# Kernel tuning notes

Measured on AMD Instinct MI355X. Metric: run time of the kernel, lower is better.

Reference implementation:

```python
import jax, jax.numpy as jnp
import numpy as np

B, S, DIN = 4, 2048, 1024
H, D = 16, 64  # num_head, per-head dim_out


def _xavier(key, shape):
    fan_in, fan_out = shape[0], shape[1]
    limit = float(np.sqrt(6.0 / (fan_in + fan_out)))
    return jax.random.uniform(key, shape, jnp.float32, -limit, limit)


def setup_inputs() -> dict:
    key = jax.random.key(0)
    k_x, k_q, k_k, k_v, k_o = jax.random.split(key, 5)
    inputs = jax.random.normal(k_x, (B, S, DIN), jnp.float32)
    # weights stored as [in, out] (transpose of torch Linear.weight); bias zeros
    return {
        "inputs": inputs,
        "wq": _xavier(k_q, (DIN, H * D)), "bq": jnp.zeros((H * D,), jnp.float32),
        "wk": _xavier(k_k, (DIN, H * D)), "bk": jnp.zeros((H * D,), jnp.float32),
        "wv": _xavier(k_v, (DIN, H * D)), "bv": jnp.zeros((H * D,), jnp.float32),
        "wo": _xavier(k_o, (H * D, D)),  "bo": jnp.zeros((D,), jnp.float32),
    }


def reference(inputs, wq, bq, wk, bk, wv, bv, wo, bo):
    b, s, _ = inputs.shape
    q = (inputs @ wq + bq).reshape(b, s, H, D).transpose(0, 2, 1, 3)  # bhsd
    k = (inputs @ wk + bk).reshape(b, s, H, D).transpose(0, 2, 1, 3)
    v = (inputs @ wv + bv).reshape(b, s, H, D).transpose(0, 2, 1, 3)
    scores = jnp.einsum('bhsd,bhSd->bhsS', q, k) / jnp.sqrt(jnp.float32(D))
    p = jax.nn.softmax(scores, axis=-1)
    o = jnp.einsum('bhsS,bhSd->bhsd', p, v)
    o = o.transpose(0, 2, 1, 3).reshape(b, s, H * D)
    return o @ wo + bo  # [b, s, D]
```

## Files before the change

kernel.cpp:

```cpp
#include <hip/hip_runtime.h>

typedef __attribute__((ext_vector_type(8))) __bf16 bf16x8;
typedef __attribute__((ext_vector_type(4))) float f32x4;

#define NB   4
#define NS   2048
#define NDIN 1024
#define NH   16
#define ND   64
#define NHD  1024
#define NM   (NB * NS)

__device__ __forceinline__ float bf2f(unsigned short u) {
    unsigned int x = ((unsigned int)u) << 16;
    return __builtin_bit_cast(float, x);
}
__device__ __forceinline__ unsigned short f2bf(float f) {
    unsigned int u = __builtin_bit_cast(unsigned int, f);
    u += 0x7fff + ((u >> 16) & 1);
    return (unsigned short)(u >> 16);
}
__device__ __forceinline__ unsigned int cvt_pk_bf16(float lo, float hi) {
    unsigned int r;
    asm("v_cvt_pk_bf16_f32 %0, %1, %2" : "=v"(r) : "v"(lo), "v"(hi));
    return r;
}
__device__ __forceinline__ void gload16(const unsigned short* g, unsigned short* l) {
    __builtin_amdgcn_global_load_lds((const __attribute__((address_space(1))) unsigned int*)g,
                                     (__attribute__((address_space(3))) unsigned int*)l, 16, 0, 0);
}

__global__ __launch_bounds__(256) void prep(
    const float* __restrict__ X, const float* __restrict__ wq,
    const float* __restrict__ wk, const float* __restrict__ wv,
    const float* __restrict__ wo, unsigned short* __restrict__ Xb,
    unsigned short* __restrict__ Wt, unsigned short* __restrict__ WoT) {
    __shared__ unsigned short t[32][33];
    int blk = blockIdx.x, tid = threadIdx.x;
    if (blk < 4096) {
        int i = blk * 256 + tid;
        float4 a = ((const float4*)X)[i * 2];
        float4 b = ((const float4*)X)[i * 2 + 1];
        union { uint4 u; unsigned short s[8]; } o;
        o.s[0] = f2bf(a.x); o.s[1] = f2bf(a.y); o.s[2] = f2bf(a.z); o.s[3] = f2bf(a.w);
        o.s[4] = f2bf(b.x); o.s[5] = f2bf(b.y); o.s[6] = f2bf(b.z); o.s[7] = f2bf(b.w);
        *(uint4*)(Xb + (size_t)i * 8) = o.u;
    } else if (blk < 4096 + 3072) {
        int bb = blk - 4096;
        int z = bb >> 10, rem = bb & 1023;
        const float* src = z == 0 ? wq : z == 1 ? wk : wv;
        unsigned short* dst = Wt + (size_t)z * 1024 * 1024;
        int k0 = (rem & 31) * 32, n0 = (rem >> 5) * 32;
        int tx = tid & 31, ty = tid >> 5;
#pragma unroll
        for (int i = 0; i < 32; i += 8)
            t[ty + i][tx] = f2bf(src[(size_t)(k0 + ty + i) * 1024 + (n0 + tx)]);
        __syncthreads();
#pragma unroll
        for (int i = 0; i < 32; i += 8)
            dst[(size_t)(n0 + ty + i) * 1024 + (k0 + tx)] = t[tx][ty + i];
    } else {
        int bb = blk - 7168;
        int k0 = (bb & 31) * 32, n0 = (bb >> 5) * 32;
        int tx = tid & 31, ty = tid >> 5;
#pragma unroll
        for (int i = 0; i < 32; i += 8)
            t[ty + i][tx] = f2bf(wo[(size_t)(k0 + ty + i) * 64 + (n0 + tx)]);
        __syncthreads();
#pragma unroll
        for (int i = 0; i < 32; i += 8)
            WoT[(size_t)(n0 + ty + i) * 1024 + (k0 + tx)] = t[tx][ty + i];
    }
}

__global__ __launch_bounds__(256) void gemm_qkv(
    const unsigned short* __restrict__ X, const unsigned short* __restrict__ Wt,
    const float* __restrict__ bq, const float* __restrict__ bk,
    const float* __restrict__ bv,
    unsigned short* __restrict__ Q, unsigned short* __restrict__ K,
    unsigned short* __restrict__ V) {
    __shared__ unsigned short smem[16384];

    int lin = blockIdx.x;
    int xcd = lin & 7, ii = lin >> 3;
    int mt = xcd * 8 + (ii & 7);
    int nt = ii >> 3;
    int mb = mt * 128, nb = nt * 128;

    int tid = threadIdx.x;
    int wid = tid >> 6, lane = tid & 63, quad = lane >> 4, l16 = lane & 15;
    int wm = (wid & 1) * 64, wn = (wid >> 1) * 64;

    int srow = 16 * wid + (lane >> 2);
    int scol = (lane & 3) * 8;
    const unsigned short* pa0 = X + (size_t)(mb + srow) * NDIN + scol;
    const unsigned short* pa1 = pa0 + (size_t)64 * NDIN;
    const unsigned short* pb0 = Wt + (size_t)(nb + srow) * NDIN + scol;
    const unsigned short* pb1 = pb0 + (size_t)64 * NDIN;

    auto stage = [&](int buf) {
        unsigned short* la = smem + buf * 8192 + wid * 512;
        unsigned short* lb = smem + buf * 8192 + 4096 + wid * 512;
        gload16(pa0, la);
        gload16(pa1, la + 2048);
        gload16(pb0, lb);
        gload16(pb1, lb + 2048);
        pa0 += 32; pa1 += 32; pb0 += 32; pb1 += 32;
    };

    f32x4 acc[4][4];
#pragma unroll
    for (int i = 0; i < 4; i++)
#pragma unroll
        for (int j = 0; j < 4; j++) acc[i][j] = (f32x4){0.f, 0.f, 0.f, 0.f};

    stage(0);
    __syncthreads();
    int cur = 0;
    for (int k0 = 0; k0 < NDIN; k0 += 32) {
        if (k0 + 32 < NDIN) stage(cur ^ 1);
        const unsigned short* Ab = smem + cur * 8192;
        const unsigned short* Bb = Ab + 4096;
        bf16x8 af[4], bfr[4];
#pragma unroll
        for (int i = 0; i < 4; i++)
            af[i] = *(const bf16x8*)(Ab + (wm + i * 16 + l16) * 32 + quad * 8);
#pragma unroll
        for (int j = 0; j < 4; j++)
            bfr[j] = *(const bf16x8*)(Bb + (wn + j * 16 + l16) * 32 + quad * 8);
#pragma unroll
        for (int i = 0; i < 4; i++)
#pragma unroll
            for (int j = 0; j < 4; j++)
                acc[i][j] = __builtin_amdgcn_mfma_f32_16x16x32_bf16(af[i], bfr[j], acc[i][j], 0, 0, 0);
        __syncthreads();
        cur ^= 1;
    }

    unsigned short (*Cl)[128] = (unsigned short (*)[128])smem;
    int wsel = nb >> 10;
    const float* bias = (wsel == 0) ? bq : (wsel == 1) ? bk : bv;
    unsigned short* dstp = (wsel == 0) ? Q : (wsel == 1) ? K : V;
#pragma unroll
    for (int i = 0; i < 4; i++)
#pragma unroll
        for (int j = 0; j < 4; j++) {
            int nl = wn + j * 16 + l16;
            float bias_v = bias[(nb & 1023) + nl];
#pragma unroll
            for (int r = 0; r < 4; r++) {
                int ml = wm + i * 16 + quad * 4 + r;
                int pc = ((nl >> 3) ^ (ml & 15));
                Cl[ml][(pc << 3) | (nl & 7)] = f2bf(acc[i][j][r] + bias_v);
            }
        }
    __syncthreads();
    {
        int hl = tid >> 7, sl = tid & 127;
        int h = ((nb & 1023) >> 6) + hl;
        int m = mb + sl, b = m >> 11, sidx = m & 2047;
        unsigned short* orow = dstp + ((size_t)((b * NH + h) * NS + sidx)) * ND;
#pragma unroll
        for (int c = 0; c < 8; c++) {
            int pc = ((hl * 8 + c) ^ (sl & 15));
            *(uint4*)(orow + c * 8) = *(const uint4*)(&Cl[sl][pc << 3]);
        }
    }
}

__global__ __launch_bounds__(256) void attn(
    const unsigned short* __restrict__ Q, const unsigned short* __restrict__ K,
    const unsigned short* __restrict__ V, unsigned short* __restrict__ Obuf) {
    __shared__ unsigned short Kl[2][64][64];
    __shared__ unsigned short Vt[2][64][64];

    int lin = blockIdx.x;
    int xcd = lin & 7, idx = lin >> 3;
    int bh = ((idx >> 4) << 3) | xcd;
    int qt = idx & 15;

    size_t base = (size_t)bh * NS * ND;
    int tid = threadIdx.x, wid = tid >> 6, lane = tid & 63;
    int quad = lane >> 4, l16 = lane & 15;
    int lx = l16 & 7;
    int q0 = qt * 128 + wid * 32;

    bf16x8 qa[2][2];
#pragma unroll
    for (int s = 0; s < 2; s++)
#pragma unroll
        for (int f = 0; f < 2; f++) {
            union { uint4 u; unsigned short sv[8]; } in_, out_;
            in_.u = *(const uint4*)(Q + base + (size_t)(q0 + s * 16 + l16) * ND + f * 32 + quad * 8);
#pragma unroll
            for (int j = 0; j < 8; j++) out_.sv[j] = f2bf(bf2f(in_.sv[j]) * 0.125f);
            qa[s][f] = __builtin_bit_cast(bf16x8, out_.u);
        }

    float lrow[2] = {0.f, 0.f};
    f32x4 o[2][4];
#pragma unroll
    for (int s = 0; s < 2; s++)
#pragma unroll
        for (int t = 0; t < 4; t++) o[s][t] = (f32x4){0.f, 0.f, 0.f, 0.f};

    int c0 = tid, c1 = tid + 256;
    int kr0w = c0 >> 3, kc0 = c0 & 7, kg0c = kc0 ^ (kr0w & 7);
    int kr1w = c1 >> 3, kc1 = c1 & 7, kg1c = kc1 ^ (kr1w & 7);
    const unsigned short* kp0 = K + base + (size_t)kr0w * ND + kc0 * 8;
    const unsigned short* kp1 = K + base + (size_t)kr1w * ND + kc1 * 8;
    int p = tid & 31, dqA = tid >> 5, dqB = dqA + 8;
    int cp = ((p >> 4) << 2) | ((p >> 1) & 3);
    int ps = (((p >> 3) & 1) << 2) | ((p & 1) << 1);
    int cb = cp ^ ((dqA & 1) << 2);
    const unsigned short* vg = V + base + (size_t)(2 * p) * ND + dqA * 4;

    uint4 k0r, k1r;
    uint2 va0, va1, va2, va3;

    auto loadRegs = [&]() {
        k0r = *(const uint4*)kp0;
        k1r = *(const uint4*)kp1;
        va0 = *(const uint2*)(vg);
        va1 = *(const uint2*)(vg + ND);
        va2 = *(const uint2*)(vg + 32);
        va3 = *(const uint2*)(vg + ND + 32);
    };
    auto bump = [&]() { kp0 += 64 * ND; kp1 += 64 * ND; vg += 64 * ND; };

    auto writeKV = [&](int buf) {
        *(uint4*)(&Kl[buf][kr0w][kg0c * 8]) = k0r;
        *(uint4*)(&Kl[buf][kr1w][kg1c * 8]) = k1r;
        unsigned short* vt = &Vt[buf][0][0];
        unsigned int w0 = __builtin_amdgcn_perm(va1.x, va0.x, 0x05040100u);
        unsigned int w1 = __builtin_amdgcn_perm(va1.x, va0.x, 0x07060302u);
        unsigned int w2 = __builtin_amdgcn_perm(va1.y, va0.y, 0x05040100u);
        unsigned int w3 = __builtin_amdgcn_perm(va1.y, va0.y, 0x07060302u);
        *(unsigned int*)(vt + (dqA * 4 + 0) * 64 + ((cb ^ 0) << 3) + ps) = w0;
        *(unsigned int*)(vt + (dqA * 4 + 1) * 64 + ((cb ^ 1) << 3) + ps) = w1;
        *(unsigned int*)(vt + (dqA * 4 + 2) * 64 + ((cb ^ 2) << 3) + ps) = w2;
        *(unsigned int*)(vt + (dqA * 4 + 3) * 64 + ((cb ^ 3) << 3) + ps) = w3;
        unsigned int x0 = __builtin_amdgcn_perm(va3.x, va2.x, 0x05040100u);
        unsigned int x1 = __builtin_amdgcn_perm(va3.x, va2.x, 0x07060302u);
        unsigned int x2 = __builtin_amdgcn_perm(va3.y, va2.y, 0x05040100u);
        unsigned int x3 = __builtin_amdgcn_perm(va3.y, va2.y, 0x07060302u);
        *(unsigned int*)(vt + (dqB * 4 + 0) * 64 + ((cb ^ 0) << 3) + ps) = x0;
        *(unsigned int*)(vt + (dqB * 4 + 1) * 64 + ((cb ^ 1) << 3) + ps) = x1;
        *(unsigned int*)(vt + (dqB * 4 + 2) * 64 + ((cb ^ 2) << 3) + ps) = x2;
        *(unsigned int*)(vt + (dqB * 4 + 3) * 64 + ((cb ^ 3) << 3) + ps) = x3;
    };

    f32x4 st[2][4];
    bf16x8 pbA[2][2], pbB[2][2];

    auto QKT = [&](int nb_) {
#pragma unroll
        for (int sub = 0; sub < 4; sub++) {
            bf16x8 kb0 = *(const bf16x8*)(&Kl[nb_][sub * 16 + l16][((quad ^ lx) << 3)]);
            bf16x8 kb1 = *(const bf16x8*)(&Kl[nb_][sub * 16 + l16][(((4 + quad) ^ lx) << 3)]);
#pragma unroll
            for (int s = 0; s < 2; s++) {
                f32x4 c = (f32x4){0.f, 0.f, 0.f, 0.f};
                c = __builtin_amdgcn_mfma_f32_16x16x32_bf16(kb0, qa[s][0], c, 0, 0, 0);
                c = __builtin_amdgcn_mfma_f32_16x16x32_bf16(kb1, qa[s][1], c, 0, 0, 0);
                st[s][sub] = c;
            }
        }
    };
    auto SM = [&](bf16x8 (&pbP)[2][2]) {
#pragma unroll
        for (int s = 0; s < 2; s++) {
            float sum = 0.f;
#pragma unroll
            for (int sub = 0; sub < 4; sub++)
#pragma unroll
                for (int r = 0; r < 4; r++) {
                    float pv = __expf(st[s][sub][r]);
                    st[s][sub][r] = pv;
                    sum += pv;
                }
            lrow[s] += sum;
            unsigned int a0 = cvt_pk_bf16(st[s][0][0], st[s][0][1]);
            unsigned int a1 = cvt_pk_bf16(st[s][0][2], st[s][0][3]);
            unsigned int a2 = cvt_pk_bf16(st[s][1][0], st[s][1][1]);
            unsigned int a3 = cvt_pk_bf16(st[s][1][2], st[s][1][3]);
            pbP[s][0] = __builtin_bit_cast(bf16x8, (uint4){a0, a1, a2, a3});
            unsigned int b0 = cvt_pk_bf16(st[s][2][0], st[s][2][1]);
            unsigned int b1 = cvt_pk_bf16(st[s][2][2], st[s][2][3]);
            unsigned int b2 = cvt_pk_bf16(st[s][3][0], st[s][3][1]);
            unsigned int b3 = cvt_pk_bf16(st[s][3][2], st[s][3][3]);
            pbP[s][1] = __builtin_bit_cast(bf16x8, (uint4){b0, b1, b2, b3});
        }
    };
    auto PV = [&](int cb_, bf16x8 (&pbC)[2][2]) {
#pragma unroll
        for (int t = 0; t < 4; t++) {
            bf16x8 vb0 = *(const bf16x8*)(&Vt[cb_][t * 16 + l16][((quad ^ lx) << 3)]);
            bf16x8 vb1 = *(const bf16x8*)(&Vt[cb_][t * 16 + l16][(((4 + quad) ^ lx) << 3)]);
#pragma unroll
            for (int s = 0; s < 2; s++) {
                o[s][t] = __builtin_amdgcn_mfma_f32_16x16x32_bf16(vb0, pbC[s][0], o[s][t], 0, 0, 0);
                o[s][t] = __builtin_amdgcn_mfma_f32_16x16x32_bf16(vb1, pbC[s][1], o[s][t], 0, 0, 0);
            }
        }
    };

    auto body = [&](int cb_, int nb_, bf16x8 (&pbC)[2][2], bf16x8 (&pbP)[2][2], bool more) {
        if (more) { bump(); loadRegs(); }
        __builtin_amdgcn_s_setprio(1);
        QKT(nb_);
        PV(cb_, pbC);
        __builtin_amdgcn_s_setprio(0);
        SM(pbP);
        __syncthreads();
        if (more) writeKV(cb_);
        __syncthreads();
    };

    loadRegs();
    writeKV(0);
    bump(); loadRegs();
    writeKV(1);
    __syncthreads();
    QKT(0);
    SM(pbA);

    for (int it = 0; it < 15; ++it) {
        body(0, 1, pbA, pbB, true);
        body(1, 0, pbB, pbA, true);
    }
    body(0, 1, pbA, pbB, false);
    __builtin_amdgcn_s_setprio(1);
    PV(1, pbB);
    __builtin_amdgcn_s_setprio(0);

    int b = bh >> 4, h = bh & 15;
#pragma unroll
    for (int s = 0; s < 2; s++) {
        float ls = lrow[s];
        ls += __shfl_xor(ls, 16, 64);
        ls += __shfl_xor(ls, 32, 64);
        float inv = 1.0f / ls;
        int q = q0 + s * 16 + l16;
#pragma unroll
        for (int t = 0; t < 4; t++) {
            uint2 w;
            w.x = cvt_pk_bf16(o[s][t][0] * inv, o[s][t][1] * inv);
            w.y = cvt_pk_bf16(o[s][t][2] * inv, o[s][t][3] * inv);
            *(uint2*)(Obuf + (size_t)(b * NS + q) * NHD + h * ND + t * 16 + quad * 4) = w;
        }
    }
}

__global__ __launch_bounds__(256) void out_proj(
    const unsigned short* __restrict__ Obuf, const unsigned short* __restrict__ WoT,
    const float* __restrict__ bo, float* __restrict__ Out) {
    __shared__ float red[4][16][64];
    int m0 = blockIdx.x * 16;
    int tid = threadIdx.x, wid = tid >> 6, lane = tid & 63;
    int quad = lane >> 4, l16 = lane & 15;
    f32x4 acc[4];
#pragma unroll
    for (int t = 0; t < 4; t++) acc[t] = (f32x4){0.f, 0.f, 0.f, 0.f};
    int kb = wid * 256;
    for (int k0 = kb; k0 < kb + 256; k0 += 32) {
        bf16x8 a = *(const bf16x8*)(Obuf + (size_t)(m0 + l16) * NHD + k0 + quad * 8);
#pragma unroll
        for (int t = 0; t < 4; t++) {
            bf16x8 b = *(const bf16x8*)(WoT + (size_t)(t * 16 + l16) * NHD + k0 + quad * 8);
            acc[t] = __builtin_amdgcn_mfma_f32_16x16x32_bf16(a, b, acc[t], 0, 0, 0);
        }
    }
#pragma unroll
    for (int t = 0; t < 4; t++)
#pragma unroll
        for (int r = 0; r < 4; r++) red[wid][t * 4 + r][lane] = acc[t][r];
    __syncthreads();
    if (tid < 64) {
        int q2 = tid >> 4, s16 = tid & 15;
#pragma unroll
        for (int t = 0; t < 4; t++) {
            int n = t * 16 + s16;
            float bb = bo[n];
#pragma unroll
            for (int r = 0; r < 4; r++) {
                int idx = t * 4 + r;
                float v = red[0][idx][tid] + red[1][idx][tid] + red[2][idx][tid] + red[3][idx][tid];
                int m = m0 + q2 * 4 + r;
                Out[(size_t)m * ND + n] = v + bb;
            }
        }
    }
}

extern "C" void kernel_launch(void* const* d_in, const int* in_sizes, int n_in,
                              void* d_out, int out_size, void* d_ws, size_t ws_size,
                              hipStream_t stream) {
    const float* X  = (const float*)d_in[0];
    const float* wq = (const float*)d_in[1];
    const float* bq = (const float*)d_in[2];
    const float* wk = (const float*)d_in[3];
    const float* bk = (const float*)d_in[4];
    const float* wv = (const float*)d_in[5];
    const float* bv = (const float*)d_in[6];
    const float* wo = (const float*)d_in[7];
    const float* bo = (const float*)d_in[8];
    float* Out = (float*)d_out;

    char* w = (char*)d_ws;
    unsigned short* Wt  = (unsigned short*)w; w += (size_t)3072 * 1024 * 2;
    unsigned short* WoT = (unsigned short*)w; w += (size_t)64 * 1024 * 2;
    unsigned short* Xb  = (unsigned short*)w; w += (size_t)NM * NDIN * 2;
    unsigned short* Qb  = (unsigned short*)w; w += (size_t)NM * NHD * 2;
    unsigned short* Kb  = (unsigned short*)w; w += (size_t)NM * NHD * 2;
    unsigned short* Vb  = (unsigned short*)w; w += (size_t)NM * NHD * 2;
    unsigned short* Ob  = (unsigned short*)w; w += (size_t)NM * NHD * 2;

    prep<<<7232, 256, 0, stream>>>(X, wq, wk, wv, wo, Xb, Wt, WoT);
    gemm_qkv<<<1536, 256, 0, stream>>>(Xb, Wt, bq, bk, bv, Qb, Kb, Vb);
    attn<<<1024, 256, 0, stream>>>(Qb, Kb, Vb, Ob);
    out_proj<<<512, 256, 0, stream>>>(Ob, WoT, bo, Out);
}
```

Before: 272.7 us.

## Store V transposed from projection GEMM and async-load K/V tiles in attention

The QKV projection epilogue now writes V in a transposed [b,h,d,s] layout, so the attention kernel no longer has to permute V through registers before writing it to shared memory. The attention kernel replaces register-staged K/V loads with direct global-to-LDS loads (gload16) into pre-swizzled double buffers. The software-pipelined QK/PV interleave, which overlapped the previous tile's PV with the next QK, is dropped in favour of a simpler per-tile loop. This removes VALU permute work and register pressure but loses the cross-iteration MFMA/softmax overlap.

```diff
diff --git a/kernel.cpp b/kernel.cpp
--- a/kernel.cpp
+++ b/kernel.cpp
@@ -139,23 +139,23 @@
 
     unsigned short (*Cl)[128] = (unsigned short (*)[128])smem;
     int wsel = nb >> 10;
-    const float* bias = (wsel == 0) ? bq : (wsel == 1) ? bk : bv;
-    unsigned short* dstp = (wsel == 0) ? Q : (wsel == 1) ? K : V;
-#pragma unroll
-    for (int i = 0; i < 4; i++)
-#pragma unroll
-        for (int j = 0; j < 4; j++) {
-            int nl = wn + j * 16 + l16;
-            float bias_v = bias[(nb & 1023) + nl];
-#pragma unroll
-            for (int r = 0; r < 4; r++) {
-                int ml = wm + i * 16 + quad * 4 + r;
-                int pc = ((nl >> 3) ^ (ml & 15));
-                Cl[ml][(pc << 3) | (nl & 7)] = f2bf(acc[i][j][r] + bias_v);
+    if (wsel < 2) {
+        const float* bias = (wsel == 0) ? bq : bk;
+        unsigned short* dstp = (wsel == 0) ? Q : K;
+#pragma unroll
+        for (int i = 0; i < 4; i++)
+#pragma unroll
+            for (int j = 0; j < 4; j++) {
+                int nl = wn + j * 16 + l16;
+                float bias_v = bias[(nb & 1023) + nl];
+#pragma unroll
+                for (int r = 0; r < 4; r++) {
+                    int ml = wm + i * 16 + quad * 4 + r;
+                    int pc = ((nl >> 3) ^ (ml & 15));
+                    Cl[ml][(pc << 3) | (nl & 7)] = f2bf(acc[i][j][r] + bias_v);
+                }
             }
-        }
-    __syncthreads();
-    {
+        __syncthreads();
         int hl = tid >> 7, sl = tid & 127;
         int h = ((nb & 1023) >> 6) + hl;
         int m = mb + sl, b = m >> 11, sidx = m & 2047;
@@ -165,12 +165,38 @@
             int pc = ((hl * 8 + c) ^ (sl & 15));
             *(uint4*)(orow + c * 8) = *(const uint4*)(&Cl[sl][pc << 3]);
         }
+    } else {
+#pragma unroll
+        for (int i = 0; i < 4; i++)
+#pragma unroll
+            for (int j = 0; j < 4; j++) {
+                int nl = wn + j * 16 + l16;
+                float bias_v = bv[(nb & 1023) + nl];
+#pragma unroll
+                for (int r = 0; r < 4; r++) {
+                    int pml = wm + (i >> 1) * 32 + quad * 8 + (i & 1) * 4 + r;
+                    int pc = ((pml >> 3) ^ (nl & 15));
+                    Cl[nl][(pc << 3) | (pml & 7)] = f2bf(acc[i][j][r] + bias_v);
+                }
+            }
+        __syncthreads();
+        int b = mb >> 11, smb = mb & 2047;
+        int h0 = (nb & 1023) >> 6;
+#pragma unroll
+        for (int c = 0; c < 8; c++) {
+            int o = c * 256 + tid;
+            int row = o >> 4, sc = o & 15;
+            int pc = sc ^ (row & 15);
+            uint4 v = *(const uint4*)(&Cl[row][pc << 3]);
+            int h = h0 + (row >> 6), d = row & 63;
+            *(uint4*)(V + ((size_t)((b * NH + h) * ND + d)) * NS + smb + sc * 8) = v;
+        }
     }
 }
 
 __global__ __launch_bounds__(256) void attn(
     const unsigned short* __restrict__ Q, const unsigned short* __restrict__ K,
-    const unsigned short* __restrict__ V, unsigned short* __restrict__ Obuf) {
+    const unsigned short* __restrict__ VT, unsigned short* __restrict__ Obuf) {
     __shared__ unsigned short Kl[2][64][64];
     __shared__ unsigned short Vt[2][64][64];
 
@@ -204,60 +230,40 @@
 #pragma unroll
         for (int t = 0; t < 4; t++) o[s][t] = (f32x4){0.f, 0.f, 0.f, 0.f};
 
-    int c0 = tid, c1 = tid + 256;
-    int kr0w = c0 >> 3, kc0 = c0 & 7, kg0c = kc0 ^ (kr0w & 7);
-    int kr1w = c1 >> 3, kc1 = c1 & 7, kg1c = kc1 ^ (kr1w & 7);
-    const unsigned short* kp0 = K + base + (size_t)kr0w * ND + kc0 * 8;
-    const unsigned short* kp1 = K + base + (size_t)kr1w * ND + kc1 * 8;
-    int p = tid & 31, dqA = tid >> 5, dqB = dqA + 8;
-    int cp = ((p >> 4) << 2) | ((p >> 1) & 3);
-    int ps = (((p >> 3) & 1) << 2) | ((p & 1) << 1);
-    int cb = cp ^ ((dqA & 1) << 2);
-    const unsigned short* vg = V + base + (size_t)(2 * p) * ND + dqA * 4;
-
-    uint4 k0r, k1r;
-    uint2 va0, va1, va2, va3;
-
-    auto loadRegs = [&]() {
-        k0r = *(const uint4*)kp0;
-        k1r = *(const uint4*)kp1;
-        va0 = *(const uint2*)(vg);
-        va1 = *(const uint2*)(vg + ND);
-        va2 = *(const uint2*)(vg + 32);
-        va3 = *(const uint2*)(vg + ND + 32);
+    int r0 = wid * 16 + (lane >> 3), r1 = r0 + 8;
+    int p0 = lane & 7;
+    const unsigned short* kp0 = K + base + (size_t)r0 * ND + ((p0 ^ (r0 & 7)) * 8);
+    const unsigned short* kp1 = K + base + (size_t)r1 * ND + ((p0 ^ (r1 & 7)) * 8);
+    const unsigned short* vp0 = VT + base + (size_t)r0 * NS + ((p0 ^ (r0 & 7)) * 8);
+    const unsigned short* vp1 = VT + base + (size_t)r1 * NS + ((p0 ^ (r1 & 7)) * 8);
+
+    auto stageKV = [&](int buf) {
+        unsigned short* kb = &Kl[buf][0][0] + wid * 1024;
+        unsigned short* vb = &Vt[buf][0][0] + wid * 1024;
+        gload16(kp0, kb);
+        gload16(kp1, kb + 512);
+        gload16(vp0, vb);
+        gload16(vp1, vb + 512);
     };
-    auto bump = [&]() { kp0 += 64 * ND; kp1 += 64 * ND; vg += 64 * ND; };
-
-    auto writeKV = [&](int buf) {
-        *(uint4*)(&Kl[buf][kr0w][kg0c * 8]) = k0r;
-        *(uint4*)(&Kl[buf][kr1w][kg1c * 8]) = k1r;
-        unsigned short* vt = &Vt[buf][0][0];
-        unsigned int w0 = __builtin_amdgcn_perm(va1.x, va0.x, 0x05040100u);
-        unsigned int w1 = __builtin_amdgcn_perm(va1.x, va0.x, 0x07060302u);
-        unsigned int w2 = __builtin_amdgcn_perm(va1.y, va0.y, 0x05040100u);
-        unsigned int w3 = __builtin_amdgcn_perm(va1.y, va0.y, 0x07060302u);
-        *(unsigned int*)(vt + (dqA * 4 + 0) * 64 + ((cb ^ 0) << 3) + ps) = w0;
-        *(unsigned int*)(vt + (dqA * 4 + 1) * 64 + ((cb ^ 1) << 3) + ps) = w1;
-        *(unsigned int*)(vt + (dqA * 4 + 2) * 64 + ((cb ^ 2) << 3) + ps) = w2;
-        *(unsigned int*)(vt + (dqA * 4 + 3) * 64 + ((cb ^ 3) << 3) + ps) = w3;
-        unsigned int x0 = __builtin_amdgcn_perm(va3.x, va2.x, 0x05040100u);
-        unsigned int x1 = __builtin_amdgcn_perm(va3.x, va2.x, 0x07060302u);
-        unsigned int x2 = __builtin_amdgcn_perm(va3.y, va2.y, 0x05040100u);
-        unsigned int x3 = __builtin_amdgcn_perm(va3.y, va2.y, 0x07060302u);
-        *(unsigned int*)(vt + (dqB * 4 + 0) * 64 + ((cb ^ 0) << 3) + ps) = x0;
-        *(unsigned int*)(vt + (dqB * 4 + 1) * 64 + ((cb ^ 1) << 3) + ps) = x1;
-        *(unsigned int*)(vt + (dqB * 4 + 2) * 64 + ((cb ^ 2) << 3) + ps) = x2;
-        *(unsigned int*)(vt + (dqB * 4 + 3) * 64 + ((cb ^ 3) << 3) + ps) = x3;
-    };
-
-    f32x4 st[2][4];
-    bf16x8 pbA[2][2], pbB[2][2];
-
-    auto QKT = [&](int nb_) {
+
+    stageKV(0);
+    __syncthreads();
+
+    int cur = 0;
+    for (int kc = 0; kc < NS; kc += 64) {
+        bool more = (kc + 64 < NS);
+        if (more) {
+            kp0 += 64 * ND; kp1 += 64 * ND; vp0 += 64; vp1 += 64;
+            stageKV(cur ^ 1);
+        }
+
+        f32x4 st[2][4];
+        __builtin_amdgcn_s_setprio(1);
 #pragma unroll
         for (int sub = 0; sub < 4; sub++) {
-            bf16x8 kb0 = *(const bf16x8*)(&Kl[nb_][sub * 16 + l16][((quad ^ lx) << 3)]);
-            bf16x8 kb1 = *(const bf16x8*)(&Kl[nb_][sub * 16 + l16][(((4 + quad) ^ lx) << 3)]);
+            const unsigned short* kr = &Kl[cur][sub * 16 + l16][0];
+            bf16x8 kb0 = *(const bf16x8*)(kr + ((quad ^ lx) << 3));
+            bf16x8 kb1 = *(const bf16x8*)(kr + (((4 + quad) ^ lx) << 3));
 #pragma unroll
             for (int s = 0; s < 2; s++) {
                 f32x4 c = (f32x4){0.f, 0.f, 0.f, 0.f};
@@ -266,8 +272,9 @@
                 st[s][sub] = c;
             }
         }
-    };
-    auto SM = [&](bf16x8 (&pbP)[2][2]) {
+        __builtin_amdgcn_s_setprio(0);
+
+        bf16x8 pb[2][2];
 #pragma unroll
         for (int s = 0; s < 2; s++) {
             float sum = 0.f;
@@ -284,55 +291,31 @@
             unsigned int a1 = cvt_pk_bf16(st[s][0][2], st[s][0][3]);
             unsigned int a2 = cvt_pk_bf16(st[s][1][0], st[s][1][1]);
             unsigned int a3 = cvt_pk_bf16(st[s][1][2], st[s][1][3]);
-            pbP[s][0] = __builtin_bit_cast(bf16x8, (uint4){a0, a1, a2, a3});
+            pb[s][0] = __builtin_bit_cast(bf16x8, (uint4){a0, a1, a2, a3});
             unsigned int b0 = cvt_pk_bf16(st[s][2][0], st[s][2][1]);
             unsigned int b1 = cvt_pk_bf16(st[s][2][2], st[s][2][3]);
             unsigned int b2 = cvt_pk_bf16(st[s][3][0], st[s][3][1]);
             unsigned int b3 = cvt_pk_bf16(st[s][3][2], st[s][3][3]);
-            pbP[s][1] = __builtin_bit_cast(bf16x8, (uint4){b0, b1, b2, b3});
-        }
-    };
-    auto PV = [&](int cb_, bf16x8 (&pbC)[2][2]) {
+            pb[s][1] = __builtin_bit_cast(bf16x8, (uint4){b0, b1, b2, b3});
+        }
+
+        __builtin_amdgcn_s_setprio(1);
 #pragma unroll
         for (int t = 0; t < 4; t++) {
-            bf16x8 vb0 = *(const bf16x8*)(&Vt[cb_][t * 16 + l16][((quad ^ lx) << 3)]);
-            bf16x8 vb1 = *(const bf16x8*)(&Vt[cb_][t * 16 + l16][(((4 + quad) ^ lx) << 3)]);
+            const unsigned short* vr = &Vt[cur][t * 16 + l16][0];
+            bf16x8 vb0 = *(const bf16x8*)(vr + ((quad ^ lx) << 3));
+            bf16x8 vb1 = *(const bf16x8*)(vr + (((4 + quad) ^ lx) << 3));
 #pragma unroll
             for (int s = 0; s < 2; s++) {
-                o[s][t] = __builtin_amdgcn_mfma_f32_16x16x32_bf16(vb0, pbC[s][0], o[s][t], 0, 0, 0);
-                o[s][t] = __builtin_amdgcn_mfma_f32_16x16x32_bf16(vb1, pbC[s][1], o[s][t], 0, 0, 0);
+                o[s][t] = __builtin_amdgcn_mfma_f32_16x16x32_bf16(vb0, pb[s][0], o[s][t], 0, 0, 0);
+                o[s][t] = __builtin_amdgcn_mfma_f32_16x16x32_bf16(vb1, pb[s][1], o[s][t], 0, 0, 0);
             }
         }
-    };
-
-    auto body = [&](int cb_, int nb_, bf16x8 (&pbC)[2][2], bf16x8 (&pbP)[2][2], bool more) {
-        if (more) { bump(); loadRegs(); }
-        __builtin_amdgcn_s_setprio(1);
-        QKT(nb_);
-        PV(cb_, pbC);
         __builtin_amdgcn_s_setprio(0);
-        SM(pbP);
-        __syncthreads();
-        if (more) writeKV(cb_);
-        __syncthreads();
-    };
-
-    loadRegs();
-    writeKV(0);
-    bump(); loadRegs();
-    writeKV(1);
-    __syncthreads();
-    QKT(0);
-    SM(pbA);
-
-    for (int it = 0; it < 15; ++it) {
-        body(0, 1, pbA, pbB, true);
-        body(1, 0, pbB, pbA, true);
-    }
-    body(0, 1, pbA, pbB, false);
-    __builtin_amdgcn_s_setprio(1);
-    PV(1, pbB);
-    __builtin_amdgcn_s_setprio(0);
+
+        __syncthreads();
+        cur ^= 1;
+    }
 
     int b = bh >> 4, h = bh & 15;
 #pragma unroll
```

Measured after the change: 280.6 us. 2.9% more time.
